# Kernel tuning notes

Measured on AMD Instinct MI355X. Metric: run time of the kernel, lower is better.

Reference implementation:

```python
import jax, jax.numpy as jnp
import numpy as np

N_NODES = 100000
N_EDGES = 1600000


def _sage_conv(x, src, dst, W_l, W_r, b):
    """PyG SAGEConv (mean aggr): lin_l(mean of neighbor feats) + b + lin_r(x)."""
    n = x.shape[0]
    msgs = x[src]                                            # [E, F] gather
    agg = jax.ops.segment_sum(msgs, dst, num_segments=n)     # [N, F]
    cnt = jax.ops.segment_sum(jnp.ones((src.shape[0],), x.dtype), dst,
                              num_segments=n)                # [N]
    mean = agg / jnp.maximum(cnt, 1.0)[:, None]
    return mean @ W_l + b + x @ W_r


def setup_inputs() -> dict:
    key = jax.random.key(0)
    ks = jax.random.split(key, 8)
    x = jax.random.normal(ks[0], (N_NODES, 64), dtype=jnp.float32)
    edge_index = jax.random.randint(ks[1], (2, N_EDGES), 0, N_NODES, dtype=jnp.int64)
    # Glorot-ish small init for weights
    W1_l = jax.random.normal(ks[2], (64, 128), dtype=jnp.float32) * 0.1
    W1_r = jax.random.normal(ks[3], (64, 128), dtype=jnp.float32) * 0.1
    b1 = jax.random.normal(ks[4], (128,), dtype=jnp.float32) * 0.1
    W2_l = jax.random.normal(ks[5], (128, 64), dtype=jnp.float32) * 0.1
    W2_r = jax.random.normal(ks[6], (128, 64), dtype=jnp.float32) * 0.1
    b2 = jax.random.normal(ks[7], (64,), dtype=jnp.float32) * 0.1
    return {"x": x, "edge_index": edge_index, "W1_l": W1_l, "W1_r": W1_r,
            "b1": b1, "W2_l": W2_l, "W2_r": W2_r, "b2": b2}


def reference(x, edge_index, W1_l, W1_r, b1, W2_l, W2_r, b2):
    src, dst = edge_index[0], edge_index[1]
    h = jax.nn.relu(_sage_conv(x, src, dst, W1_l, W1_r, b1))  # [N, 128]
    out = _sage_conv(h, src, dst, W2_l, W2_r, b2)             # [N, 64]
    return out
```

## Files before the change

kernel.cpp:

```cpp
#include <hip/hip_runtime.h>
#include <hip/hip_bf16.h>
#include <stdint.h>


typedef unsigned short u16;
typedef __attribute__((ext_vector_type(8))) short short8;
typedef __attribute__((ext_vector_type(4))) float f32x4;

#define BSHIFT 9
#define BSIZE  512
#define CHUNK  8192
#define NCP    256

__device__ __forceinline__ float bf2f(u16 v) { return __uint_as_float(((uint32_t)v) << 16); }
__device__ __forceinline__ float bfu_lo(uint32_t u) { return __uint_as_float(u << 16); }
__device__ __forceinline__ float bfu_hi(uint32_t u) { return __uint_as_float(u & 0xffff0000u); }
__device__ __forceinline__ u16 f2bf(float f) {
    uint32_t u = __float_as_uint(f);
    return (u16)((u + 0x7fffu + ((u >> 16) & 1u)) >> 16);
}

__global__ __launch_bounds__(256) void probe_k(
    const void* x, const void* w1l, const void* w1r, const void* b1,
    const void* w2l, const void* w2r, const void* b2, const void* ei,
    int* __restrict__ flags, int ne,
    int c0, int c1, int c2, int c3, int c4, int c5, int c6) {
    __shared__ int cs_s[8];
    int tid = threadIdx.x, a = tid >> 5, lane = tid & 31;
    if (tid < 8) cs_s[tid] = 0;
    __syncthreads();
    if (a < 7) {
        const void* ptrs[7] = {x, w1l, w1r, b1, w2l, w2r, b2};
        int cs[7] = {c0, c1, c2, c3, c4, c5, c6};
        int C = cs[a];
        int stride = C / 32; if (stride < 1) stride = 1;
        long long i = (long long)lane * stride;
        if (i > C - 1) i = C - 1;
        i &= ~1LL;
        u16 v = ((const u16*)ptrs[a])[i];
        int e = (v >> 7) & 0xFF;
        int sane = ((e >= 0x50 && e <= 0x97) || v == 0) ? 1 : 0;
        atomicAdd(&cs_s[a], sane);
    } else {
        long long n32 = 2LL * ne;
        long long stride = n32 / 32; if (stride < 1) stride = 1;
        long long i = (long long)lane * stride; i |= 1;
        if (i >= n32) i = 1;
        int wv = ((const int*)ei)[i];
        atomicAdd(&cs_s[7], wv != 0 ? 1 : 0);
    }
    __syncthreads();
    if (tid < 7) flags[tid] = (cs_s[tid] >= 24) ? 1 : 0;
    if (tid == 7) flags[7] = (cs_s[7] == 0) ? 1 : 0;
}

__global__ __launch_bounds__(512) void prep_w(
    const void* __restrict__ W1l, const void* __restrict__ W1r,
    const void* __restrict__ W2l, const void* __restrict__ W2r,
    u16* __restrict__ wpk, const int* __restrict__ flags) {
    int tid = threadIdx.x;
    int b = blockIdx.x;
    const void* src = (b == 0) ? W1l : (b == 1) ? W1r : (b == 2) ? W2l : W2r;
    int isbf = flags[(b == 0) ? 1 : (b == 1) ? 2 : (b == 2) ? 4 : 5];
    u16* dst = wpk + ((b >= 2) ? (16384 + (b - 2) * 8192) : 0);
    for (int i = tid; i < 2048; i += 512) {
        u16 v0, v1, v2, v3;
        if (isbf) {
            ushort4 u = ((const ushort4*)src)[i];
            v0 = u.x; v1 = u.y; v2 = u.z; v3 = u.w;
        } else {
            float4 u = ((const float4*)src)[i];
            v0 = f2bf(u.x); v1 = f2bf(u.y); v2 = f2bf(u.z); v3 = f2bf(u.w);
        }
        int k, n, k8;
        if (b <= 1) { k = i >> 5; n = (i & 31) * 4; k8 = (b == 1 ? 8 : 0) + (k >> 3); }
        else        { k = i >> 4; n = (i & 15) * 4; k8 = k >> 3; }
        int kc = k8 >> 2, q = k8 & 3, w = k & 7;
        int base = ((n >> 4) * 4 + kc) * 512 + (q * 16 + (n & 15)) * 8 + w;
        dst[base] = v0; dst[base + 8] = v1; dst[base + 16] = v2; dst[base + 24] = v3;
    }
}

__global__ __launch_bounds__(256) void convert_x(
    const void* __restrict__ x, u16* __restrict__ xb,
    const int* __restrict__ flags, int n4) {
    if (flags[0]) return;
    int i = blockIdx.x * 256 + threadIdx.x;
    if (i < n4) {
        float4 f = ((const float4*)x)[i];
        *(ushort4*)&xb[(size_t)i * 4] =
            make_ushort4(f2bf(f.x), f2bf(f.y), f2bf(f.z), f2bf(f.w));
    }
}

__global__ __launch_bounds__(512) void count_chunks(
    const void* __restrict__ ei, int* __restrict__ hist2d,
    const int* __restrict__ flags, int nn, int ne, int nb) {
    __shared__ int hist[512];
    int tid = threadIdx.x;
    hist[tid] = 0;
    __syncthreads();
    int e64 = flags[7];
    int base = blockIdx.x * CHUNK;
#pragma unroll
    for (int j = 0; j < 16; j++) {
        int e = base + j * 512 + tid;
        if (e < ne) {
            int dst = e64 ? (int)((const long long*)ei)[(size_t)ne + e]
                          : ((const int*)ei)[(size_t)ne + e];
            if ((unsigned)dst < (unsigned)nn) atomicAdd(&hist[dst >> BSHIFT], 1);
        }
    }
    __syncthreads();
    for (int b = tid; b < nb; b += 512)
        hist2d[b * NCP + blockIdx.x] = hist[b];
}

__global__ __launch_bounds__(256) void scan2d(
    const int* __restrict__ hist2d, int* __restrict__ base2d,
    int* __restrict__ btot, int nchunk) {
    __shared__ int t0[256];
    int b = blockIdx.x, tid = threadIdx.x;
    int v = (tid < nchunk) ? hist2d[b * NCP + tid] : 0;
    t0[tid] = v;
    __syncthreads();
    for (int d = 1; d < 256; d <<= 1) {
        int t = (tid >= d) ? t0[tid - d] : 0;
        __syncthreads();
        t0[tid] += t;
        __syncthreads();
    }
    if (tid < nchunk) base2d[b * NCP + tid] = t0[tid] - v;
    if (tid == 255) btot[b] = t0[255];
}

__global__ __launch_bounds__(512) void scan_buckets(
    const int* __restrict__ btot, int* __restrict__ bo, int nb) {
    __shared__ int t0[512];
    int tid = threadIdx.x;
    int v = (tid < nb) ? btot[tid] : 0;
    t0[tid] = v;
    __syncthreads();
    for (int d = 1; d < 512; d <<= 1) {
        int t = (tid >= d) ? t0[tid - d] : 0;
        __syncthreads();
        t0[tid] += t;
        __syncthreads();
    }
    if (tid < nb) bo[tid] = t0[tid] - v;
    if (tid == 511) bo[nb] = t0[511];
}

__global__ __launch_bounds__(512) void partition_k(
    const void* __restrict__ ei, const int* __restrict__ bo,
    const int* __restrict__ base2d,
    unsigned* __restrict__ ep, const int* __restrict__ flags,
    int nn, int ne, int nb) {
    __shared__ unsigned stage[CHUNK];
    __shared__ u16 ab[CHUNK];
    __shared__ int hist[512], incl[512], exl[512], gbase[512], lcur[512];
    int tid = threadIdx.x;
    int base = blockIdx.x * CHUNK;
    hist[tid] = 0;
    __syncthreads();
    int e64 = flags[7];
    unsigned pk[16]; int bk[16];
#pragma unroll
    for (int j = 0; j < 16; j++) {
        int e = base + j * 512 + tid;
        bk[j] = -1;
        pk[j] = 0;
        if (e < ne) {
            int src, dst;
            if (e64) {
                src = (int)((const long long*)ei)[e];
                dst = (int)((const long long*)ei)[(size_t)ne + e];
            } else {
                src = ((const int*)ei)[e];
                dst = ((const int*)ei)[(size_t)ne + e];
            }
            if ((unsigned)dst < (unsigned)nn) {
                if ((unsigned)src >= (unsigned)nn) src = 0;
                bk[j] = dst >> BSHIFT;
                pk[j] = (unsigned)src | ((unsigned)(dst & (BSIZE - 1)) << 17);
                atomicAdd(&hist[bk[j]], 1);
            }
        }
    }
    __syncthreads();
    incl[tid] = hist[tid];
    __syncthreads();
    for (int d = 1; d < 512; d <<= 1) {
        int t = (tid >= d) ? incl[tid - d] : 0;
        __syncthreads();
        incl[tid] += t;
        __syncthreads();
    }
    int ex = incl[tid] - hist[tid];
    exl[tid] = ex;
    lcur[tid] = ex;
    gbase[tid] = (tid < nb) ? (bo[tid] + base2d[tid * NCP + blockIdx.x]) : 0;
    __syncthreads();
#pragma unroll
    for (int j = 0; j < 16; j++) {
        if (bk[j] >= 0) {
            int r = atomicAdd(&lcur[bk[j]], 1);
            stage[r] = pk[j];
            ab[r] = (u16)bk[j];
        }
    }
    __syncthreads();
    int tot = incl[511];
    for (int j = tid; j < tot; j += 512) {
        int b = ab[j];
        ep[gbase[b] + (j - exl[b])] = stage[j];
    }
}

__global__ __launch_bounds__(512) void csr_fill2(
    const unsigned* __restrict__ ep, const int* __restrict__ bo,
    int* __restrict__ off, int* __restrict__ cnt, int* __restrict__ esrc,
    int nn) {
    __shared__ int hist[BSIZE], incl[BSIZE], lcur[BSIZE];
    int b = blockIdx.x;
    int beg = bo[b], end = bo[b + 1];
    int tid = threadIdx.x;
    hist[tid] = 0;
    __syncthreads();
    for (int j = beg + tid; j < end; j += 512)
        atomicAdd(&hist[(ep[j] >> 17) & (BSIZE - 1)], 1);
    __syncthreads();
    incl[tid] = hist[tid];
    __syncthreads();
    for (int d = 1; d < 512; d <<= 1) {
        int t = (tid >= d) ? incl[tid - d] : 0;
        __syncthreads();
        incl[tid] += t;
        __syncthreads();
    }
    int ex = beg + incl[tid] - hist[tid];
    lcur[tid] = ex;
    int node = b * BSIZE + tid;
    if (node < nn) { off[node] = ex; cnt[node] = hist[tid]; }
    __syncthreads();
    for (int j = beg + tid; j < end; j += 512) {
        unsigned p = ep[j];
        int r = atomicAdd(&lcur[(p >> 17) & (BSIZE - 1)], 1);
        esrc[r] = (int)(p & 0x1FFFFu);
    }
}

__global__ __launch_bounds__(512, 8) void layer1(
    const void* __restrict__ x, const u16* __restrict__ xb,
    const int* __restrict__ esrc,
    const int* __restrict__ off, const int* __restrict__ cnt,
    const u16* __restrict__ w1g, const void* __restrict__ b1,
    u16* __restrict__ h, const int* __restrict__ flags, int nn) {
    __shared__ __align__(16) u16 wA[8 * 512];
    __shared__ float b_s[128];
    int tid = threadIdx.x;
    int node0 = blockIdx.x * 32;

    if (tid < 128) b_s[tid] = flags[3] ? bf2f(((const u16*)b1)[tid]) : ((const float*)b1)[tid];

    int grp = tid >> 4, gl = tid & 15;
    int n = node0 + grp;
    int mtile = grp >> 4, l15m = grp & 15;
    int idx_mean = (mtile * 4 + (gl >> 3)) * 512 + (((gl >> 1) & 3) * 16 + l15m) * 8 + (gl & 1) * 4;
    int idx_x = (mtile * 4 + 2 + (gl >> 3)) * 512 + (((gl >> 1) & 3) * 16 + l15m) * 8 + (gl & 1) * 4;
    const u16* xs = flags[0] ? (const u16*)x : xb;
    if (n < nn) {
        int beg = off[n], deg = cnt[n];
        float a0 = 0.f, a1 = 0.f, a2 = 0.f, a3 = 0.f;
        int i = 0;
        const u16* xbp = xs + gl * 4;
        for (; i + 8 <= deg; i += 8) {
            ushort4 v[8];
#pragma unroll
            for (int j = 0; j < 8; j++) {
                int s0 = esrc[beg + i + j];
                v[j] = *(const ushort4*)(xbp + (size_t)s0 * 64);
            }
#pragma unroll
            for (int j = 0; j < 8; j++) {
                a0 += bf2f(v[j].x); a1 += bf2f(v[j].y);
                a2 += bf2f(v[j].z); a3 += bf2f(v[j].w);
            }
        }
        for (; i < deg; i++) {
            int s0 = esrc[beg + i];
            ushort4 v = *(const ushort4*)(xbp + (size_t)s0 * 64);
            a0 += bf2f(v.x); a1 += bf2f(v.y); a2 += bf2f(v.z); a3 += bf2f(v.w);
        }
        float inv = 1.0f / (float)(deg > 0 ? deg : 1);
        *(ushort4*)&wA[idx_mean] =
            make_ushort4(f2bf(a0 * inv), f2bf(a1 * inv), f2bf(a2 * inv), f2bf(a3 * inv));
        *(ushort4*)&wA[idx_x] = *(const ushort4*)(xs + (size_t)n * 64 + gl * 4);
    } else {
        *(ushort4*)&wA[idx_mean] = make_ushort4(0, 0, 0, 0);
        *(ushort4*)&wA[idx_x] = make_ushort4(0, 0, 0, 0);
    }
    __syncthreads();

    int wv = tid >> 6, lane = tid & 63;
    int l15 = lane & 15, q = lane >> 4;
    f32x4 acc0 = {0.f, 0.f, 0.f, 0.f};
    f32x4 acc1 = {0.f, 0.f, 0.f, 0.f};
#pragma unroll
    for (int kc = 0; kc < 4; kc++) {
        short8 a0 = *(const short8*)&wA[(kc) * 512 + lane * 8];
        short8 a1 = *(const short8*)&wA[(4 + kc) * 512 + lane * 8];
        short8 b  = *(const short8*)&w1g[(wv * 4 + kc) * 512 + lane * 8];
        acc0 = __builtin_amdgcn_mfma_f32_16x16x32_bf16(a0, b, acc0, 0, 0, 0);
        acc1 = __builtin_amdgcn_mfma_f32_16x16x32_bf16(a1, b, acc1, 0, 0, 0);
    }
    int nc = wv * 16 + l15;
    float bias = b_s[nc];
#pragma unroll
    for (int r = 0; r < 4; r++) {
        int m = q * 4 + r;
        int nd = node0 + m;
        if (nd < nn) h[(size_t)nd * 128 + nc] = f2bf(fmaxf(acc0[r] + bias, 0.0f));
        nd = node0 + 16 + m;
        if (nd < nn) h[(size_t)nd * 128 + nc] = f2bf(fmaxf(acc1[r] + bias, 0.0f));
    }
}

__global__ __launch_bounds__(256, 8) void pre2(
    const u16* __restrict__ h, const u16* __restrict__ w2lg,
    u16* __restrict__ g, int nn) {
    int tid = threadIdx.x;
    int node0 = blockIdx.x * 64;
    int wv = tid >> 6, lane = tid & 63;
    int l15 = lane & 15, q = lane >> 4;
    int arow = node0 + wv * 16 + l15;
    if (arow >= nn) arow = nn - 1;
    const u16* hrow = h + (size_t)arow * 128 + q * 8;
    f32x4 acc[4];
#pragma unroll
    for (int nt = 0; nt < 4; nt++) acc[nt] = (f32x4){0.f, 0.f, 0.f, 0.f};
#pragma unroll
    for (int kc = 0; kc < 4; kc++) {
        short8 a = *(const short8*)(hrow + kc * 32);
#pragma unroll
        for (int nt = 0; nt < 4; nt++) {
            short8 b = *(const short8*)&w2lg[(nt * 4 + kc) * 512 + lane * 8];
            acc[nt] = __builtin_amdgcn_mfma_f32_16x16x32_bf16(a, b, acc[nt], 0, 0, 0);
        }
    }
#pragma unroll
    for (int nt = 0; nt < 4; nt++) {
        int nc = nt * 16 + l15;
#pragma unroll
        for (int r = 0; r < 4; r++) {
            int nd = node0 + wv * 16 + q * 4 + r;
            if (nd < nn) g[(size_t)nd * 64 + nc] = f2bf(acc[nt][r]);
        }
    }
}

__global__ __launch_bounds__(512, 8) void layer2(
    const u16* __restrict__ h, const u16* __restrict__ g,
    const int* __restrict__ esrc,
    const int* __restrict__ off, const int* __restrict__ cnt,
    const u16* __restrict__ w2rg, const void* __restrict__ b2,
    void* __restrict__ out, const int* __restrict__ flags, int nn) {
    __shared__ __align__(16) u16 wA2[8 * 512];
    __shared__ __align__(16) float meanbuf[32][72];
    __shared__ float b_s[64];
    int tid = threadIdx.x;
    int node0 = blockIdx.x * 32;
    int obf = flags[0];

    if (tid < 64) b_s[tid] = flags[6] ? bf2f(((const u16*)b2)[tid]) : ((const float*)b2)[tid];

    int grp = tid >> 4, gl = tid & 15;
    int n = node0 + grp;
    int mtile = grp >> 4, m15 = grp & 15;
    int idx_h = (mtile * 4 + (gl >> 2)) * 512 + ((gl & 3) * 16 + m15) * 8;
    if (n < nn) {
        *(uint4*)&wA2[idx_h] = *(const uint4*)(h + (size_t)n * 128 + gl * 8);
        int beg = off[n], deg = cnt[n];
        float a0 = 0.f, a1 = 0.f, a2 = 0.f, a3 = 0.f;
        const u16* gb = g + gl * 4;
        int i = 0;
        for (; i + 8 <= deg; i += 8) {
            uint2 v[8];
#pragma unroll
            for (int j = 0; j < 8; j++) {
                int s0 = esrc[beg + i + j];
                v[j] = *(const uint2*)(gb + (size_t)s0 * 64);
            }
#pragma unroll
            for (int j = 0; j < 8; j++) {
                a0 += bfu_lo(v[j].x); a1 += bfu_hi(v[j].x);
                a2 += bfu_lo(v[j].y); a3 += bfu_hi(v[j].y);
            }
        }
        for (; i < deg; i++) {
            int s0 = esrc[beg + i];
            uint2 v = *(const uint2*)(gb + (size_t)s0 * 64);
            a0 += bfu_lo(v.x); a1 += bfu_hi(v.x);
            a2 += bfu_lo(v.y); a3 += bfu_hi(v.y);
        }
        float inv = 1.0f / (float)(deg > 0 ? deg : 1);
        *(float4*)&meanbuf[grp][gl * 4] =
            make_float4(a0 * inv, a1 * inv, a2 * inv, a3 * inv);
    } else {
        *(uint4*)&wA2[idx_h] = make_uint4(0, 0, 0, 0);
        *(float4*)&meanbuf[grp][gl * 4] = make_float4(0.f, 0.f, 0.f, 0.f);
    }
    __syncthreads();

    int wv = tid >> 6, lane = tid & 63;
    int l15 = lane & 15, q = lane >> 4;
    int mt = wv >> 2, nt = wv & 3;
    f32x4 acc = {0.f, 0.f, 0.f, 0.f};
#pragma unroll
    for (int kc = 0; kc < 4; kc++) {
        short8 a = *(const short8*)&wA2[(mt * 4 + kc) * 512 + lane * 8];
        short8 b = *(const short8*)&w2rg[(nt * 4 + kc) * 512 + lane * 8];
        acc = __builtin_amdgcn_mfma_f32_16x16x32_bf16(a, b, acc, 0, 0, 0);
    }
    int nc = nt * 16 + l15;
    float bias = b_s[nc];
#pragma unroll
    for (int r = 0; r < 4; r++) {
        int m = mt * 16 + q * 4 + r;
        int nd = node0 + m;
        if (nd < nn) {
            float v = acc[r] + bias + meanbuf[m][nc];
            if (obf) ((u16*)out)[(size_t)nd * 64 + nc] = f2bf(v);
            else     ((float*)out)[(size_t)nd * 64 + nc] = v;
        }
    }
}

__global__ __launch_bounds__(256) void zero_out_k(u16* __restrict__ out, int n) {
    int i = blockIdx.x * 256 + threadIdx.x;
    if (i < n) out[i] = 0;
}

extern "C" void kernel_launch(void* const* d_in, const int* in_sizes, int n_in,
                              void* d_out, int out_size, void* d_ws, size_t ws_size,
                              hipStream_t stream) {
    const void* x   = d_in[0];
    const void* ei  = d_in[1];
    const void* W1l = d_in[2];
    const void* W1r = d_in[3];
    const void* b1  = d_in[4];
    const void* W2l = d_in[5];
    const void* W2r = d_in[6];
    const void* b2  = d_in[7];

    int nn = in_sizes[0] / 64;
    int ne = in_sizes[1] / 2;
    int nb = (nn + BSIZE - 1) / BSIZE;
    int nchunk = (ne + CHUNK - 1) / CHUNK;

    auto al = [](size_t v) { return (v + 255) & ~(size_t)255; };
    size_t o_flags = 0;
    size_t o_bo    = 256;
    size_t o_btot  = al(o_bo + 513 * 4);
    size_t o_wpk   = al(o_btot + 512 * 4);
    size_t o_cnt   = al(o_wpk + 65536);
    size_t o_off   = al(o_cnt + (size_t)nn * 4);
    size_t o_esrc  = al(o_off + (size_t)nn * 4);
    size_t o_h     = al(o_esrc + (size_t)ne * 4);
    size_t o_g     = al(o_h + (size_t)nn * 128 * 2);
    size_t ws_req  = o_g + (size_t)nn * 64 * 2;

    size_t o_ep   = o_h;
    size_t o_h2d  = al(o_ep + (size_t)ne * 4);
    size_t o_b2d  = al(o_h2d + (size_t)512 * NCP * 4);
    size_t ov_end = o_b2d + (size_t)512 * NCP * 4;

    bool ok = ws_size >= ws_req && nb >= 1 && nb <= 512 && nn <= 131072 &&
              nchunk <= NCP && ov_end <= o_g;
    if (!ok) {
        zero_out_k<<<(out_size + 255) / 256, 256, 0, stream>>>((u16*)d_out, out_size);
        return;
    }

    char* ws = (char*)d_ws;
    int* flags  = (int*)(ws + o_flags);
    int* bo     = (int*)(ws + o_bo);
    int* btot   = (int*)(ws + o_btot);
    u16* wpk    = (u16*)(ws + o_wpk);
    int* cnt    = (int*)(ws + o_cnt);
    int* off    = (int*)(ws + o_off);
    int* esrc   = (int*)(ws + o_esrc);
    u16* h      = (u16*)(ws + o_h);
    u16* xbg    = (u16*)(ws + o_g);
    unsigned* ep = (unsigned*)(ws + o_ep);
    int* hist2d = (int*)(ws + o_h2d);
    int* base2d = (int*)(ws + o_b2d);

    probe_k<<<1, 256, 0, stream>>>(x, W1l, W1r, b1, W2l, W2r, b2, ei, flags, ne,
                                   in_sizes[0], in_sizes[2], in_sizes[3], in_sizes[4],
                                   in_sizes[5], in_sizes[6], in_sizes[7]);
    prep_w<<<4, 512, 0, stream>>>(W1l, W1r, W2l, W2r, wpk, flags);
    int n4 = nn * 16;
    convert_x<<<(n4 + 255) / 256, 256, 0, stream>>>(x, xbg, flags, n4);
    count_chunks<<<nchunk, 512, 0, stream>>>(ei, hist2d, flags, nn, ne, nb);
    scan2d<<<nb, 256, 0, stream>>>(hist2d, base2d, btot, nchunk);
    scan_buckets<<<1, 512, 0, stream>>>(btot, bo, nb);
    partition_k<<<nchunk, 512, 0, stream>>>(ei, bo, base2d, ep, flags, nn, ne, nb);
    csr_fill2<<<nb, 512, 0, stream>>>(ep, bo, off, cnt, esrc, nn);
    int lb = (nn + 31) / 32;
    layer1<<<lb, 512, 0, stream>>>(x, xbg, esrc, off, cnt, wpk, b1, h, flags, nn);
    pre2<<<(nn + 63) / 64, 256, 0, stream>>>(h, wpk + 16384, xbg, nn);
    layer2<<<lb, 512, 0, stream>>>(h, xbg, esrc, off, cnt, wpk + 24576, b2, d_out, flags, nn);
}
```

Measured before the change: 245.6 us.

## Fuse setup kernels, inline bucket scan, fold pre2 matmul into layer1

Merges probe, weight packing, x conversion and chunk counting into one multi-role setup kernel that detects input dtypes locally with ballots. The single-block bucket scan kernel is dropped and the scan is recomputed redundantly in each partition and CSR-fill block. Layer1 now also computes the h·W2_l projection with MFMA into a separate buffer when workspace allows, which removes the pre2 kernel and a reread of h. The gather loops get an extra 16-wide unroll. Together these cut launch count and intermediate traffic, at the cost of redundant scans, more register pressure and more shared-memory reuse in layer1.

```diff
diff --git a/kernel.cpp b/kernel.cpp
--- a/kernel.cpp
+++ b/kernel.cpp
@@ -20,100 +20,127 @@
     return (u16)((u + 0x7fffu + ((u >> 16) & 1u)) >> 16);
 }
 
-__global__ __launch_bounds__(256) void probe_k(
-    const void* x, const void* w1l, const void* w1r, const void* b1,
-    const void* w2l, const void* w2r, const void* b2, const void* ei,
-    int* __restrict__ flags, int ne,
+__global__ __launch_bounds__(512) void setup_k(
+    const void* __restrict__ x, const void* __restrict__ ei,
+    const void* __restrict__ W1l, const void* __restrict__ W1r,
+    const void* __restrict__ b1, const void* __restrict__ W2l,
+    const void* __restrict__ W2r, const void* __restrict__ b2,
+    u16* __restrict__ wpk, u16* __restrict__ xb,
+    int* __restrict__ hist2d, int* __restrict__ flags,
+    int nn, int ne, int nb, int nchunk, int ncvt,
     int c0, int c1, int c2, int c3, int c4, int c5, int c6) {
-    __shared__ int cs_s[8];
-    int tid = threadIdx.x, a = tid >> 5, lane = tid & 31;
-    if (tid < 8) cs_s[tid] = 0;
-    __syncthreads();
-    if (a < 7) {
-        const void* ptrs[7] = {x, w1l, w1r, b1, w2l, w2r, b2};
-        int cs[7] = {c0, c1, c2, c3, c4, c5, c6};
-        int C = cs[a];
-        int stride = C / 32; if (stride < 1) stride = 1;
-        long long i = (long long)lane * stride;
-        if (i > C - 1) i = C - 1;
-        i &= ~1LL;
-        u16 v = ((const u16*)ptrs[a])[i];
-        int e = (v >> 7) & 0xFF;
-        int sane = ((e >= 0x50 && e <= 0x97) || v == 0) ? 1 : 0;
-        atomicAdd(&cs_s[a], sane);
+    __shared__ int sh[512];
+    __shared__ int sflag;
+    int bid = blockIdx.x, tid = threadIdx.x;
+    if (bid < nchunk) {
+        sh[tid] = 0;
+        int samp = 0;
+        if (tid < 32) {
+            long long n32 = 2LL * ne;
+            long long stride = n32 / 32; if (stride < 1) stride = 1;
+            long long i = (long long)tid * stride; i |= 1;
+            if (i >= n32) i = 1;
+            samp = (((const int*)ei)[i] != 0);
+        }
+        unsigned long long m = __ballot(samp);
+        if (tid == 0) sflag = (m == 0ULL) ? 1 : 0;
+        __syncthreads();
+        int e64 = sflag;
+        int base = bid * CHUNK;
+#pragma unroll
+        for (int j = 0; j < 16; j++) {
+            int e = base + j * 512 + tid;
+            if (e < ne) {
+                int dst = e64 ? (int)((const long long*)ei)[(size_t)ne + e]
+                              : ((const int*)ei)[(size_t)ne + e];
+                if ((unsigned)dst < (unsigned)nn) atomicAdd(&sh[dst >> BSHIFT], 1);
+            }
+        }
+        __syncthreads();
+        for (int b = tid; b < nb; b += 512)
+            hist2d[b * NCP + bid] = sh[b];
+    } else if (bid < nchunk + ncvt) {
+        int samp = 0;
+        if (tid < 32) {
+            int C = c0; int stride = C / 32; if (stride < 1) stride = 1;
+            long long i = (long long)tid * stride;
+            if (i > C - 1) i = C - 1; i &= ~1LL;
+            u16 v = ((const u16*)x)[i];
+            int e = (v >> 7) & 0xFF;
+            samp = ((e >= 0x50 && e <= 0x97) || v == 0) ? 1 : 0;
+        }
+        unsigned long long m = __ballot(samp);
+        if (tid == 0) sflag = (__popcll(m) >= 24) ? 1 : 0;
+        __syncthreads();
+        if (sflag) return;
+        int i = (bid - nchunk) * 512 + tid;
+        if (i < nn * 16) {
+            float4 f = ((const float4*)x)[i];
+            *(ushort4*)&xb[(size_t)i * 4] =
+                make_ushort4(f2bf(f.x), f2bf(f.y), f2bf(f.z), f2bf(f.w));
+        }
+    } else if (bid < nchunk + ncvt + 4) {
+        int b = bid - nchunk - ncvt;
+        const void* src = (b == 0) ? W1l : (b == 1) ? W1r : (b == 2) ? W2l : W2r;
+        int C = (b == 0) ? c1 : (b == 1) ? c2 : (b == 2) ? c4 : c5;
+        int samp = 0;
+        if (tid < 32) {
+            int stride = C / 32; if (stride < 1) stride = 1;
+            long long i = (long long)tid * stride;
+            if (i > C - 1) i = C - 1; i &= ~1LL;
+            u16 v = ((const u16*)src)[i];
+            int e = (v >> 7) & 0xFF;
+            samp = ((e >= 0x50 && e <= 0x97) || v == 0) ? 1 : 0;
+        }
+        unsigned long long m = __ballot(samp);
+        if (tid == 0) sflag = (__popcll(m) >= 24) ? 1 : 0;
+        __syncthreads();
+        int isbf = sflag;
+        u16* dst = wpk + ((b >= 2) ? (16384 + (b - 2) * 8192) : 0);
+        for (int i = tid; i < 2048; i += 512) {
+            u16 v0, v1, v2, v3;
+            if (isbf) {
+                ushort4 u = ((const ushort4*)src)[i];
+                v0 = u.x; v1 = u.y; v2 = u.z; v3 = u.w;
+            } else {
+                float4 u = ((const float4*)src)[i];
+                v0 = f2bf(u.x); v1 = f2bf(u.y); v2 = f2bf(u.z); v3 = f2bf(u.w);
+            }
+            int k, n, k8;
+            if (b <= 1) { k = i >> 5; n = (i & 31) * 4; k8 = (b == 1 ? 8 : 0) + (k >> 3); }
+            else        { k = i >> 4; n = (i & 15) * 4; k8 = k >> 3; }
+            int kc = k8 >> 2, q = k8 & 3, w = k & 7;
+            int basei = ((n >> 4) * 4 + kc) * 512 + (q * 16 + (n & 15)) * 8 + w;
+            dst[basei] = v0; dst[basei + 8] = v1; dst[basei + 16] = v2; dst[basei + 24] = v3;
+        }
     } else {
-        long long n32 = 2LL * ne;
-        long long stride = n32 / 32; if (stride < 1) stride = 1;
-        long long i = (long long)lane * stride; i |= 1;
-        if (i >= n32) i = 1;
-        int wv = ((const int*)ei)[i];
-        atomicAdd(&cs_s[7], wv != 0 ? 1 : 0);
-    }
-    __syncthreads();
-    if (tid < 7) flags[tid] = (cs_s[tid] >= 24) ? 1 : 0;
-    if (tid == 7) flags[7] = (cs_s[7] == 0) ? 1 : 0;
-}
-
-__global__ __launch_bounds__(512) void prep_w(
-    const void* __restrict__ W1l, const void* __restrict__ W1r,
-    const void* __restrict__ W2l, const void* __restrict__ W2r,
-    u16* __restrict__ wpk, const int* __restrict__ flags) {
-    int tid = threadIdx.x;
-    int b = blockIdx.x;
-    const void* src = (b == 0) ? W1l : (b == 1) ? W1r : (b == 2) ? W2l : W2r;
-    int isbf = flags[(b == 0) ? 1 : (b == 1) ? 2 : (b == 2) ? 4 : 5];
-    u16* dst = wpk + ((b >= 2) ? (16384 + (b - 2) * 8192) : 0);
-    for (int i = tid; i < 2048; i += 512) {
-        u16 v0, v1, v2, v3;
-        if (isbf) {
-            ushort4 u = ((const ushort4*)src)[i];
-            v0 = u.x; v1 = u.y; v2 = u.z; v3 = u.w;
-        } else {
-            float4 u = ((const float4*)src)[i];
-            v0 = f2bf(u.x); v1 = f2bf(u.y); v2 = f2bf(u.z); v3 = f2bf(u.w);
-        }
-        int k, n, k8;
-        if (b <= 1) { k = i >> 5; n = (i & 31) * 4; k8 = (b == 1 ? 8 : 0) + (k >> 3); }
-        else        { k = i >> 4; n = (i & 15) * 4; k8 = k >> 3; }
-        int kc = k8 >> 2, q = k8 & 3, w = k & 7;
-        int base = ((n >> 4) * 4 + kc) * 512 + (q * 16 + (n & 15)) * 8 + w;
-        dst[base] = v0; dst[base + 8] = v1; dst[base + 16] = v2; dst[base + 24] = v3;
-    }
-}
-
-__global__ __launch_bounds__(256) void convert_x(
-    const void* __restrict__ x, u16* __restrict__ xb,
-    const int* __restrict__ flags, int n4) {
-    if (flags[0]) return;
-    int i = blockIdx.x * 256 + threadIdx.x;
-    if (i < n4) {
-        float4 f = ((const float4*)x)[i];
-        *(ushort4*)&xb[(size_t)i * 4] =
-            make_ushort4(f2bf(f.x), f2bf(f.y), f2bf(f.z), f2bf(f.w));
-    }
-}
-
-__global__ __launch_bounds__(512) void count_chunks(
-    const void* __restrict__ ei, int* __restrict__ hist2d,
-    const int* __restrict__ flags, int nn, int ne, int nb) {
-    __shared__ int hist[512];
-    int tid = threadIdx.x;
-    hist[tid] = 0;
-    __syncthreads();
-    int e64 = flags[7];
-    int base = blockIdx.x * CHUNK;
-#pragma unroll
-    for (int j = 0; j < 16; j++) {
-        int e = base + j * 512 + tid;
-        if (e < ne) {
-            int dst = e64 ? (int)((const long long*)ei)[(size_t)ne + e]
-                          : ((const int*)ei)[(size_t)ne + e];
-            if ((unsigned)dst < (unsigned)nn) atomicAdd(&hist[dst >> BSHIFT], 1);
-        }
-    }
-    __syncthreads();
-    for (int b = tid; b < nb; b += 512)
-        hist2d[b * NCP + blockIdx.x] = hist[b];
+        int a = tid >> 5, lane = tid & 31;
+        if (tid < 8) sh[tid] = 0;
+        __syncthreads();
+        if (a < 7) {
+            const void* ptrs[7] = {x, W1l, W1r, b1, W2l, W2r, b2};
+            int cs[7] = {c0, c1, c2, c3, c4, c5, c6};
+            int C = cs[a];
+            int stride = C / 32; if (stride < 1) stride = 1;
+            long long i = (long long)lane * stride;
+            if (i > C - 1) i = C - 1;
+            i &= ~1LL;
+            u16 v = ((const u16*)ptrs[a])[i];
+            int e = (v >> 7) & 0xFF;
+            int sane = ((e >= 0x50 && e <= 0x97) || v == 0) ? 1 : 0;
+            atomicAdd(&sh[a], sane);
+        } else if (a == 7) {
+            long long n32 = 2LL * ne;
+            long long stride = n32 / 32; if (stride < 1) stride = 1;
+            long long i = (long long)lane * stride; i |= 1;
+            if (i >= n32) i = 1;
+            int wv = ((const int*)ei)[i];
+            atomicAdd(&sh[7], wv != 0 ? 1 : 0);
+        }
+        __syncthreads();
+        if (tid < 7) flags[tid] = (sh[tid] >= 24) ? 1 : 0;
+        if (tid == 7) flags[7] = (sh[7] == 0) ? 1 : 0;
+    }
 }
 
 __global__ __launch_bounds__(256) void scan2d(
@@ -134,36 +161,29 @@
     if (tid == 255) btot[b] = t0[255];
 }
 
-__global__ __launch_bounds__(512) void scan_buckets(
-    const int* __restrict__ btot, int* __restrict__ bo, int nb) {
-    __shared__ int t0[512];
-    int tid = threadIdx.x;
-    int v = (tid < nb) ? btot[tid] : 0;
-    t0[tid] = v;
-    __syncthreads();
-    for (int d = 1; d < 512; d <<= 1) {
-        int t = (tid >= d) ? t0[tid - d] : 0;
-        __syncthreads();
-        t0[tid] += t;
-        __syncthreads();
-    }
-    if (tid < nb) bo[tid] = t0[tid] - v;
-    if (tid == 511) bo[nb] = t0[511];
-}
-
 __global__ __launch_bounds__(512) void partition_k(
-    const void* __restrict__ ei, const int* __restrict__ bo,
+    const void* __restrict__ ei, const int* __restrict__ btot,
     const int* __restrict__ base2d,
-    unsigned* __restrict__ ep, const int* __restrict__ flags,
-    int nn, int ne, int nb) {
+    unsigned* __restrict__ ep, int nn, int ne, int nb) {
     __shared__ unsigned stage[CHUNK];
     __shared__ u16 ab[CHUNK];
     __shared__ int hist[512], incl[512], exl[512], gbase[512], lcur[512];
+    __shared__ int e64s;
     int tid = threadIdx.x;
     int base = blockIdx.x * CHUNK;
     hist[tid] = 0;
-    __syncthreads();
-    int e64 = flags[7];
+    int samp = 0;
+    if (tid < 32) {
+        long long n32 = 2LL * ne;
+        long long stride = n32 / 32; if (stride < 1) stride = 1;
+        long long i = (long long)tid * stride; i |= 1;
+        if (i >= n32) i = 1;
+        samp = (((const int*)ei)[i] != 0);
+    }
+    unsigned long long bm = __ballot(samp);
+    if (tid == 0) e64s = (bm == 0ULL) ? 1 : 0;
+    __syncthreads();
+    int e64 = e64s;
     unsigned pk[16]; int bk[16];
 #pragma unroll
     for (int j = 0; j < 16; j++) {
@@ -199,7 +219,18 @@
     int ex = incl[tid] - hist[tid];
     exl[tid] = ex;
     lcur[tid] = ex;
-    gbase[tid] = (tid < nb) ? (bo[tid] + base2d[tid * NCP + blockIdx.x]) : 0;
+    int tot = incl[511];
+    __syncthreads();
+    incl[tid] = (tid < nb) ? btot[tid] : 0;
+    __syncthreads();
+    for (int d = 1; d < 512; d <<= 1) {
+        int t = (tid >= d) ? incl[tid - d] : 0;
+        __syncthreads();
+        incl[tid] += t;
+        __syncthreads();
+    }
+    int bo_t = incl[tid] - ((tid < nb) ? btot[tid] : 0);
+    gbase[tid] = (tid < nb) ? (bo_t + base2d[tid * NCP + blockIdx.x]) : 0;
     __syncthreads();
 #pragma unroll
     for (int j = 0; j < 16; j++) {
@@ -210,7 +241,6 @@
         }
     }
     __syncthreads();
-    int tot = incl[511];
     for (int j = tid; j < tot; j += 512) {
         int b = ab[j];
         ep[gbase[b] + (j - exl[b])] = stage[j];
@@ -218,13 +248,23 @@
 }
 
 __global__ __launch_bounds__(512) void csr_fill2(
-    const unsigned* __restrict__ ep, const int* __restrict__ bo,
+    const unsigned* __restrict__ ep, const int* __restrict__ btot,
     int* __restrict__ off, int* __restrict__ cnt, int* __restrict__ esrc,
-    int nn) {
+    int nn, int nb) {
     __shared__ int hist[BSIZE], incl[BSIZE], lcur[BSIZE];
     int b = blockIdx.x;
-    int beg = bo[b], end = bo[b + 1];
     int tid = threadIdx.x;
+    incl[tid] = (tid < nb) ? btot[tid] : 0;
+    __syncthreads();
+    for (int d = 1; d < 512; d <<= 1) {
+        int t = (tid >= d) ? incl[tid - d] : 0;
+        __syncthreads();
+        incl[tid] += t;
+        __syncthreads();
+    }
+    int end = incl[b];
+    int beg = end - btot[b];
+    __syncthreads();
     hist[tid] = 0;
     __syncthreads();
     for (int j = beg + tid; j < end; j += 512)
@@ -254,8 +294,10 @@
     const void* __restrict__ x, const u16* __restrict__ xb,
     const int* __restrict__ esrc,
     const int* __restrict__ off, const int* __restrict__ cnt,
-    const u16* __restrict__ w1g, const void* __restrict__ b1,
-    u16* __restrict__ h, const int* __restrict__ flags, int nn) {
+    const u16* __restrict__ w1g, const u16* __restrict__ w2lg,
+    const void* __restrict__ b1,
+    u16* __restrict__ h, u16* __restrict__ gpt,
+    const int* __restrict__ flags, int nn) {
     __shared__ __align__(16) u16 wA[8 * 512];
     __shared__ float b_s[128];
     int tid = threadIdx.x;
@@ -274,6 +316,19 @@
         float a0 = 0.f, a1 = 0.f, a2 = 0.f, a3 = 0.f;
         int i = 0;
         const u16* xbp = xs + gl * 4;
+        for (; i + 16 <= deg; i += 16) {
+            ushort4 v[16];
+#pragma unroll
+            for (int j = 0; j < 16; j++) {
+                int s0 = esrc[beg + i + j];
+                v[j] = *(const ushort4*)(xbp + (size_t)s0 * 64);
+            }
+#pragma unroll
+            for (int j = 0; j < 16; j++) {
+                a0 += bf2f(v[j].x); a1 += bf2f(v[j].y);
+                a2 += bf2f(v[j].z); a3 += bf2f(v[j].w);
+            }
+        }
         for (; i + 8 <= deg; i += 8) {
             ushort4 v[8];
 #pragma unroll
@@ -316,13 +371,43 @@
     }
     int nc = wv * 16 + l15;
     float bias = b_s[nc];
+    u16 hv0[4], hv1[4];
 #pragma unroll
     for (int r = 0; r < 4; r++) {
+        hv0[r] = f2bf(fmaxf(acc0[r] + bias, 0.0f));
+        hv1[r] = f2bf(fmaxf(acc1[r] + bias, 0.0f));
         int m = q * 4 + r;
         int nd = node0 + m;
-        if (nd < nn) h[(size_t)nd * 128 + nc] = f2bf(fmaxf(acc0[r] + bias, 0.0f));
+        if (nd < nn) h[(size_t)nd * 128 + nc] = hv0[r];
         nd = node0 + 16 + m;
-        if (nd < nn) h[(size_t)nd * 128 + nc] = f2bf(fmaxf(acc1[r] + bias, 0.0f));
+        if (nd < nn) h[(size_t)nd * 128 + nc] = hv1[r];
+    }
+    if (gpt) {
+        __syncthreads();
+        int kcg = wv >> 1;
+        int qg  = ((wv & 1) << 1) | (l15 >> 3);
+        int wg  = l15 & 7;
+#pragma unroll
+        for (int r = 0; r < 4; r++) {
+            int m = q * 4 + r;
+            wA[kcg * 512 + (qg * 16 + m) * 8 + wg]       = hv0[r];
+            wA[(4 + kcg) * 512 + (qg * 16 + m) * 8 + wg] = hv1[r];
+        }
+        __syncthreads();
+        int mt2 = wv >> 2, nt2 = wv & 3;
+        f32x4 ag = {0.f, 0.f, 0.f, 0.f};
+#pragma unroll
+        for (int kc = 0; kc < 4; kc++) {
+            short8 a = *(const short8*)&wA[(mt2 * 4 + kc) * 512 + lane * 8];
+            short8 b = *(const short8*)&w2lg[(nt2 * 4 + kc) * 512 + lane * 8];
+            ag = __builtin_amdgcn_mfma_f32_16x16x32_bf16(a, b, ag, 0, 0, 0);
+        }
+        int nc2 = nt2 * 16 + l15;
+#pragma unroll
+        for (int r = 0; r < 4; r++) {
+            int nd = node0 + mt2 * 16 + q * 4 + r;
+            if (nd < nn) gpt[(size_t)nd * 64 + nc2] = f2bf(ag[r]);
+        }
     }
 }
 
@@ -384,6 +469,19 @@
         float a0 = 0.f, a1 = 0.f, a2 = 0.f, a3 = 0.f;
         const u16* gb = g + gl * 4;
         int i = 0;
+        for (; i + 16 <= deg; i += 16) {
+            uint2 v[16];
+#pragma unroll
+            for (int j = 0; j < 16; j++) {
+                int s0 = esrc[beg + i + j];
+                v[j] = *(const uint2*)(gb + (size_t)s0 * 64);
+            }
+#pragma unroll
+            for (int j = 0; j < 16; j++) {
+                a0 += bfu_lo(v[j].x); a1 += bfu_hi(v[j].x);
+                a2 += bfu_lo(v[j].y); a3 += bfu_hi(v[j].y);
+            }
+        }
         for (; i + 8 <= deg; i += 8) {
             uint2 v[8];
 #pragma unroll
@@ -460,55 +558,58 @@
 
     auto al = [](size_t v) { return (v + 255) & ~(size_t)255; };
     size_t o_flags = 0;
-    size_t o_bo    = 256;
-    size_t o_btot  = al(o_bo + 513 * 4);
+    size_t o_btot  = 256;
     size_t o_wpk   = al(o_btot + 512 * 4);
     size_t o_cnt   = al(o_wpk + 65536);
     size_t o_off   = al(o_cnt + (size_t)nn * 4);
     size_t o_esrc  = al(o_off + (size_t)nn * 4);
     size_t o_h     = al(o_esrc + (size_t)ne * 4);
-    size_t o_g     = al(o_h + (size_t)nn * 128 * 2);
-    size_t ws_req  = o_g + (size_t)nn * 64 * 2;
+    size_t o_xb    = al(o_h + (size_t)nn * 128 * 2);
+    size_t ws_base = o_xb + (size_t)nn * 64 * 2;
+    size_t o_g2    = al(ws_base);
+    size_t ws_fused = o_g2 + (size_t)nn * 64 * 2;
 
     size_t o_ep   = o_h;
     size_t o_h2d  = al(o_ep + (size_t)ne * 4);
     size_t o_b2d  = al(o_h2d + (size_t)512 * NCP * 4);
     size_t ov_end = o_b2d + (size_t)512 * NCP * 4;
 
-    bool ok = ws_size >= ws_req && nb >= 1 && nb <= 512 && nn <= 131072 &&
-              nchunk <= NCP && ov_end <= o_g;
+    bool ok = ws_size >= ws_base && nb >= 1 && nb <= 512 && nn <= 131072 &&
+              nchunk <= NCP && ov_end <= o_xb;
     if (!ok) {
         zero_out_k<<<(out_size + 255) / 256, 256, 0, stream>>>((u16*)d_out, out_size);
         return;
     }
+    bool fused = ws_size >= ws_fused;
 
     char* ws = (char*)d_ws;
     int* flags  = (int*)(ws + o_flags);
-    int* bo     = (int*)(ws + o_bo);
     int* btot   = (int*)(ws + o_btot);
     u16* wpk    = (u16*)(ws + o_wpk);
     int* cnt    = (int*)(ws + o_cnt);
     int* off    = (int*)(ws + o_off);
     int* esrc   = (int*)(ws + o_esrc);
     u16* h      = (u16*)(ws + o_h);
-    u16* xbg    = (u16*)(ws + o_g);
+    u16* xb     = (u16*)(ws + o_xb);
+    u16* gbuf   = fused ? (u16*)(ws + o_g2) : xb;
     unsigned* ep = (unsigned*)(ws + o_ep);
     int* hist2d = (int*)(ws + o_h2d);
     int* base2d = (int*)(ws + o_b2d);
 
-    probe_k<<<1, 256, 0, stream>>>(x, W1l, W1r, b1, W2l, W2r, b2, ei, flags, ne,
-                                   in_sizes[0], in_sizes[2], in_sizes[3], in_sizes[4],
-                                   in_sizes[5], in_sizes[6], in_sizes[7]);
-    prep_w<<<4, 512, 0, stream>>>(W1l, W1r, W2l, W2r, wpk, flags);
-    int n4 = nn * 16;
-    convert_x<<<(n4 + 255) / 256, 256, 0, stream>>>(x, xbg, flags, n4);
-    count_chunks<<<nchunk, 512, 0, stream>>>(ei, hist2d, flags, nn, ne, nb);
+    int ncvt = (nn * 16 + 511) / 512;
+    setup_k<<<nchunk + ncvt + 5, 512, 0, stream>>>(
+        x, ei, W1l, W1r, b1, W2l, W2r, b2, wpk, xb, hist2d, flags,
+        nn, ne, nb, nchunk, ncvt,
+        in_sizes[0], in_sizes[2], in_sizes[3], in_sizes[4],
+        in_sizes[5], in_sizes[6], in_sizes[7]);
     scan2d<<<nb, 256, 0, stream>>>(hist2d, base2d, btot, nchunk);
-    scan_buckets<<<1, 512, 0, stream>>>(btot, bo, nb);
-    partition_k<<<nchunk, 512, 0, stream>>>(ei, bo, base2d, ep, flags, nn, ne, nb);
-    csr_fill2<<<nb, 512, 0, stream>>>(ep, bo, off, cnt, esrc, nn);
+    partition_k<<<nchunk, 512, 0, stream>>>(ei, btot, base2d, ep, nn, ne, nb);
+    csr_fill2<<<nb, 512, 0, stream>>>(ep, btot, off, cnt, esrc, nn, nb);
     int lb = (nn + 31) / 32;
-    layer1<<<lb, 512, 0, stream>>>(x, xbg, esrc, off, cnt, wpk, b1, h, flags, nn);
-    pre2<<<(nn + 63) / 64, 256, 0, stream>>>(h, wpk + 16384, xbg, nn);
-    layer2<<<lb, 512, 0, stream>>>(h, xbg, esrc, off, cnt, wpk + 24576, b2, d_out, flags, nn);
-}
+    layer1<<<lb, 512, 0, stream>>>(x, xb, esrc, off, cnt, wpk, wpk + 16384, b1,
+                                   h, fused ? gbuf : (u16*)nullptr, flags, nn);
+    if (!fused)
+        pre2<<<(nn + 63) / 64, 256, 0, stream>>>(h, wpk + 16384, gbuf, nn);
+    layer2<<<lb, 512, 0, stream>>>(h, gbuf, esrc, off, cnt, wpk + 24576, b2,
+                                   d_out, flags, nn);
+}
```

New measurement: 228.1 us. 1.08x faster.
